# Kernel optimization log

Hardware: AMD Instinct MI355X
Metric: run time of the kernel (lower is better)

## Reference

```python
import jax, jax.numpy as jnp
import numpy as np

B, S = 32, 8192
HE, HD = 256, 256  # encoder_hidden_size, decoder_hidden_size


def setup_inputs() -> dict:
    key = jax.random.key(0)
    ks = jax.random.split(key, 8)
    scale = 1.0 / np.sqrt(HD)
    scale_e = 1.0 / np.sqrt(HE)
    return {
        "query": jax.random.normal(ks[0], (B, 1, HD), dtype=jnp.float32),
        "keys": jax.random.normal(ks[1], (B, S, HE), dtype=jnp.float32),
        "Wa_w": jax.random.uniform(ks[2], (HD, HD), jnp.float32, -scale, scale),
        "Wa_b": jax.random.uniform(ks[3], (HD,), jnp.float32, -scale, scale),
        "Ua_w": jax.random.uniform(ks[4], (HD, HE), jnp.float32, -scale_e, scale_e),
        "Ua_b": jax.random.uniform(ks[5], (HD,), jnp.float32, -scale_e, scale_e),
        "Va_w": jax.random.uniform(ks[6], (1, HD), jnp.float32, -scale, scale),
        "Va_b": jax.random.uniform(ks[7], (1,), jnp.float32, -scale, scale),
    }


def reference(query, keys, Wa_w, Wa_b, Ua_w, Ua_b, Va_w, Va_b):
    # q_proj: [B, 1, HD]; k_proj: [B, S, HD]
    q_proj = jnp.einsum("bqd,hd->bqh", query, Wa_w) + Wa_b
    k_proj = jnp.einsum("bse,he->bsh", keys, Ua_w) + Ua_b
    # scores: [B, S] -> [B, 1, S]
    scores = jnp.einsum("bsh,h->bs", jnp.tanh(q_proj + k_proj), Va_w[0]) + Va_b[0]
    weights = jax.nn.softmax(scores, axis=-1)[:, None, :]  # [B, 1, S]
    context = jnp.einsum("bqs,bse->bqe", weights, keys)    # [B, 1, HE]
    return (context, weights)
```

## Files before the change

### kernel.cpp

```cpp
#include <hip/hip_runtime.h>
#include <hip/hip_bf16.h>
#include <stdint.h>

#define B_ 32
#define S_ 8192
#define HD_ 256
#define HE_ 256
#define CHUNK 256
#define ROWS 16
#define MSTEPS (CHUNK/ROWS)
#define NCHUNK (S_/CHUNK)

typedef __attribute__((ext_vector_type(8))) short bf16x8;
typedef __attribute__((ext_vector_type(4))) float f32x4;

__device__ __forceinline__ uint32_t cvt_pk_bf16(float lo, float hi) {
  uint32_t r;
  asm("v_cvt_pk_bf16_f32 %0, %1, %2" : "=v"(r) : "v"(lo), "v"(hi));
  return r;
}
__device__ __forceinline__ float bf2f(unsigned short h) {
  return __uint_as_float(((uint32_t)h) << 16);
}
__device__ __forceinline__ float tanh_fast(float x) {
  float e = __expf(2.0f * x);
  return 1.0f - 2.0f * __builtin_amdgcn_rcpf(e + 1.0f);
}
template<int CTRL>
__device__ __forceinline__ float dpp_shr_add(float v) {
  int t = __builtin_amdgcn_update_dpp(0, __float_as_int(v), CTRL, 0xf, 0xf, true);
  return v + __int_as_float(t);
}
__device__ __forceinline__ float row16_sum(float v) {
  v = dpp_shr_add<0x118>(v);
  v = dpp_shr_add<0x114>(v);
  v = dpp_shr_add<0x112>(v);
  v = dpp_shr_add<0x111>(v);
  return v;
}

__global__ void prep_kernel(const float* __restrict__ query,
                            const float* __restrict__ Wa_w,
                            const float* __restrict__ Wa_b,
                            const float* __restrict__ Ua_w,
                            const float* __restrict__ Ua_b,
                            float* __restrict__ qv,
                            unsigned short* __restrict__ ua_bf) {
  const int blk = blockIdx.x, t = threadIdx.x;
  if (blk < B_) {
    __shared__ float qs[HD_];
    qs[t] = query[blk * HD_ + t];
    __syncthreads();
    const float* wr = Wa_w + (size_t)t * HD_;
    float s = Wa_b[t] + Ua_b[t];
#pragma unroll 8
    for (int d = 0; d < HD_; ++d) s += qs[d] * wr[d];
    qv[blk * HD_ + t] = s;
  } else {
    const int base = (blk - B_) * 2048 + t * 8;
    float4 v0 = *(const float4*)(Ua_w + base);
    float4 v1 = *(const float4*)(Ua_w + base + 4);
    uint4 pk;
    pk.x = cvt_pk_bf16(v0.x, v0.y);
    pk.y = cvt_pk_bf16(v0.z, v0.w);
    pk.z = cvt_pk_bf16(v1.x, v1.y);
    pk.w = cvt_pk_bf16(v1.z, v1.w);
    *(uint4*)(ua_bf + base) = pk;
  }
}

__global__ __launch_bounds__(512)
__attribute__((amdgpu_waves_per_eu(4, 4)))
void main_kernel(const float* __restrict__ keys,
                 const float* __restrict__ qv,
                 const float* __restrict__ Va_w,
                 const unsigned short* __restrict__ ua_bf,
                 float* __restrict__ wexp_g,
                 float* __restrict__ partials) {
  __shared__ __align__(16) char kt[2 * ROWS * 512];
  __shared__ float sc_sum[2][16];
  __shared__ __align__(16) float num_l[8][64][4];

  const int t = threadIdx.x;
  const int b = blockIdx.y;
  const int chunk = blockIdx.x;
  const int s0 = chunk * CHUNK;
  const int lane = t & 63;
  const int w = t >> 6;
  const int ln = lane & 15;
  const int hi = lane >> 4;

  const unsigned short* ub0 = ua_bf + (size_t)(w * 32 + ln) * HE_ + hi * 8;
  const unsigned short* ub1 = ub0 + 16 * HE_;
  bf16x8 bb0[8], bb1[8];
#pragma unroll
  for (int k = 0; k < 8; ++k) {
    bb0[k] = *(const bf16x8*)(ub0 + k * 32);
    bb1[k] = *(const bf16x8*)(ub1 + k * 32);
  }
  const float q0  = qv[b * HD_ + w * 32 + ln];
  const float q1  = qv[b * HD_ + w * 32 + 16 + ln];
  const float va0 = Va_w[w * 32 + ln];
  const float va1 = Va_w[w * 32 + 16 + ln];

  const int srow = t >> 5;
  const int scch = t & 31;
  const float* ksrc = keys + ((size_t)b * S_ + s0 + srow) * HE_ + scch * 8;
  const int ldsoff = srow * 512 + ((scch * 16) ^ ((srow & 7) << 4));

  if (t < 32) ((float*)sc_sum)[t] = 0.f;
  {
    float4 a0 = *(const float4*)(ksrc);
    float4 a1 = *(const float4*)(ksrc + 4);
    uint4 pk;
    pk.x = cvt_pk_bf16(a0.x, a0.y);
    pk.y = cvt_pk_bf16(a0.z, a0.w);
    pk.z = cvt_pk_bf16(a1.x, a1.y);
    pk.w = cvt_pk_bf16(a1.z, a1.w);
    *(uint4*)(kt + ldsoff) = pk;
  }
  __syncthreads();

  const int asw = (ln & 7) << 4;
  const int nsw = (w & 7) << 4;
  float num4[4] = {0.f, 0.f, 0.f, 0.f};

  for (int i = 0; i < MSTEPS; ++i) {
    char* cur = kt + (i & 1) * (ROWS * 512);
    char* nxt = kt + ((i + 1) & 1) * (ROWS * 512);

    float4 ga0, ga1;
    if (i + 1 < MSTEPS) {
      const float* kA = ksrc + (size_t)(i + 1) * ROWS * HE_;
      ga0 = *(const float4*)(kA);
      ga1 = *(const float4*)(kA + 4);
    }

    f32x4 a00 = {0.f,0.f,0.f,0.f}, a01 = {0.f,0.f,0.f,0.f};
    const char* arow = cur + ln * 512;
#pragma unroll
    for (int k = 0; k < 8; ++k) {
      bf16x8 af = *(const bf16x8*)(arow + ((k * 64 + hi * 16) ^ asw));
      a00 = __builtin_amdgcn_mfma_f32_16x16x32_bf16(af, bb0[k], a00, 0, 0, 0);
      a01 = __builtin_amdgcn_mfma_f32_16x16x32_bf16(af, bb1[k], a01, 0, 0, 0);
    }

#pragma unroll
    for (int r = 0; r < 4; ++r) {
      float v = tanh_fast(a00[r] + q0) * va0 + tanh_fast(a01[r] + q1) * va1;
      v = row16_sum(v);
      if (ln == 15) atomicAdd(&sc_sum[i & 1][hi * 4 + r], v);
    }
    __syncthreads();

    const float e0 = __expf(sc_sum[i & 1][w]);
    const float e8 = __expf(sc_sum[i & 1][w + 8]);
    if (lane == 0) {
      float* wg = wexp_g + (size_t)b * S_ + s0 + i * ROWS;
      wg[w] = e0;
      wg[w + 8] = e8;
    }
    if (t < 16) sc_sum[(i + 1) & 1][t] = 0.f;

    {
      uint2 kv0 = *(const uint2*)(cur + w * 512 + ((lane * 8) ^ nsw));
      uint2 kv1 = *(const uint2*)(cur + (w + 8) * 512 + ((lane * 8) ^ nsw));
      num4[0] += e0 * bf2f((unsigned short)(kv0.x & 0xffff)) + e8 * bf2f((unsigned short)(kv1.x & 0xffff));
      num4[1] += e0 * bf2f((unsigned short)(kv0.x >> 16))    + e8 * bf2f((unsigned short)(kv1.x >> 16));
      num4[2] += e0 * bf2f((unsigned short)(kv0.y & 0xffff)) + e8 * bf2f((unsigned short)(kv1.y & 0xffff));
      num4[3] += e0 * bf2f((unsigned short)(kv0.y >> 16))    + e8 * bf2f((unsigned short)(kv1.y >> 16));
    }

    if (i + 1 < MSTEPS) {
      uint4 pk;
      pk.x = cvt_pk_bf16(ga0.x, ga0.y);
      pk.y = cvt_pk_bf16(ga0.z, ga0.w);
      pk.z = cvt_pk_bf16(ga1.x, ga1.y);
      pk.w = cvt_pk_bf16(ga1.z, ga1.w);
      *(uint4*)(nxt + ldsoff) = pk;
    }
    __syncthreads();
  }

  *(float4*)&num_l[w][lane][0] = make_float4(num4[0], num4[1], num4[2], num4[3]);
  __syncthreads();
  if (t < 256) {
    float s = 0.f;
#pragma unroll
    for (int ww = 0; ww < 8; ++ww) s += num_l[ww][t >> 2][t & 3];
    partials[((size_t)b * NCHUNK + chunk) * 256 + t] = s;
  }
}

__global__ void combine_kernel(const float* __restrict__ wexp_g,
                               const float* __restrict__ partials,
                               float* __restrict__ out) {
  __shared__ float red[4];
  __shared__ float rdsh;
  const int b = blockIdx.x, t = threadIdx.x;
  const float* we = wexp_g + (size_t)b * S_;
  float s = 0.f;
#pragma unroll 4
  for (int i = t; i < S_; i += 256) s += we[i];
#pragma unroll
  for (int mm = 32; mm; mm >>= 1) s += __shfl_xor(s, mm, 64);
  if ((t & 63) == 0) red[t >> 6] = s;
  __syncthreads();
  if (t == 0) rdsh = 1.0f / (red[0] + red[1] + red[2] + red[3]);
  __syncthreads();
  const float rd = rdsh;

  const float* pb = partials + (size_t)b * NCHUNK * 256;
  float num = 0.f;
#pragma unroll 4
  for (int i = 0; i < NCHUNK; ++i) num += pb[i * 256 + t];
  out[b * HE_ + t] = num * rd;

  float* wout = out + B_ * HE_ + (size_t)b * S_;
#pragma unroll 4
  for (int i = t; i < S_; i += 256) wout[i] = we[i] * rd;
}

extern "C" void kernel_launch(void* const* d_in, const int* in_sizes, int n_in,
                              void* d_out, int out_size, void* d_ws, size_t ws_size,
                              hipStream_t stream) {
  const float* query = (const float*)d_in[0];
  const float* keys  = (const float*)d_in[1];
  const float* Wa_w  = (const float*)d_in[2];
  const float* Wa_b  = (const float*)d_in[3];
  const float* Ua_w  = (const float*)d_in[4];
  const float* Ua_b  = (const float*)d_in[5];
  const float* Va_w  = (const float*)d_in[6];
  float* out = (float*)d_out;

  char* ws = (char*)d_ws;
  float* qv             = (float*)ws;
  unsigned short* ua_bf = (unsigned short*)(ws + 32 * 1024);
  float* wexp_g         = (float*)(ws + 160 * 1024);
  float* partials       = (float*)(ws + 160 * 1024 + 1048576);

  prep_kernel<<<64, 256, 0, stream>>>(query, Wa_w, Wa_b, Ua_w, Ua_b, qv, ua_bf);
  dim3 g(NCHUNK, B_);
  main_kernel<<<g, 512, 0, stream>>>(keys, qv, Va_w, ua_bf, wexp_g, partials);
  combine_kernel<<<B_, 256, 0, stream>>>(wexp_g, partials, out);
}
```

Measured before the change: 85.00 us.

## Halve main kernel block to 4 waves, each covering 64 hidden columns

The main kernel now runs 256 threads (4 waves) per block instead of 512. Each wave holds four B-fragment sets (64 hidden units) in registers and issues four MFMAs per k-step. Each thread loads two key rows per step, and each wave handles four rows in the context accumulation. The aim is to amortise each LDS A-fragment read over more MFMAs and cut per-block sync overhead, at the cost of higher register pressure (64 bf16x8 B registers) and possibly lower occupancy.

```diff
diff --git a/kernel.cpp b/kernel.cpp
--- a/kernel.cpp
+++ b/kernel.cpp
@@ -69,8 +69,7 @@
   }
 }
 
-__global__ __launch_bounds__(512)
-__attribute__((amdgpu_waves_per_eu(4, 4)))
+__global__ __launch_bounds__(256, 2)
 void main_kernel(const float* __restrict__ keys,
                  const float* __restrict__ qv,
                  const float* __restrict__ Va_w,
@@ -79,7 +78,7 @@
                  float* __restrict__ partials) {
   __shared__ __align__(16) char kt[2 * ROWS * 512];
   __shared__ float sc_sum[2][16];
-  __shared__ __align__(16) float num_l[8][64][4];
+  __shared__ __align__(16) float num_l[4][64][4];
 
   const int t = threadIdx.x;
   const int b = blockIdx.y;
@@ -90,85 +89,109 @@
   const int ln = lane & 15;
   const int hi = lane >> 4;
 
-  const unsigned short* ub0 = ua_bf + (size_t)(w * 32 + ln) * HE_ + hi * 8;
-  const unsigned short* ub1 = ub0 + 16 * HE_;
-  bf16x8 bb0[8], bb1[8];
+  const unsigned short* ub = ua_bf + (size_t)(w * 64 + ln) * HE_ + hi * 8;
+  bf16x8 bb0[8], bb1[8], bb2[8], bb3[8];
 #pragma unroll
   for (int k = 0; k < 8; ++k) {
-    bb0[k] = *(const bf16x8*)(ub0 + k * 32);
-    bb1[k] = *(const bf16x8*)(ub1 + k * 32);
-  }
-  const float q0  = qv[b * HD_ + w * 32 + ln];
-  const float q1  = qv[b * HD_ + w * 32 + 16 + ln];
-  const float va0 = Va_w[w * 32 + ln];
-  const float va1 = Va_w[w * 32 + 16 + ln];
+    bb0[k] = *(const bf16x8*)(ub + k * 32);
+    bb1[k] = *(const bf16x8*)(ub + 16 * HE_ + k * 32);
+    bb2[k] = *(const bf16x8*)(ub + 32 * HE_ + k * 32);
+    bb3[k] = *(const bf16x8*)(ub + 48 * HE_ + k * 32);
+  }
+  const int hbase = b * HD_ + w * 64 + ln;
+  const float q0  = qv[hbase];
+  const float q1  = qv[hbase + 16];
+  const float q2  = qv[hbase + 32];
+  const float q3  = qv[hbase + 48];
+  const float va0 = Va_w[w * 64 + ln];
+  const float va1 = Va_w[w * 64 + 16 + ln];
+  const float va2 = Va_w[w * 64 + 32 + ln];
+  const float va3 = Va_w[w * 64 + 48 + ln];
 
   const int srow = t >> 5;
   const int scch = t & 31;
-  const float* ksrc = keys + ((size_t)b * S_ + s0 + srow) * HE_ + scch * 8;
-  const int ldsoff = srow * 512 + ((scch * 16) ^ ((srow & 7) << 4));
+  const float* ksrcA = keys + ((size_t)b * S_ + s0 + srow) * HE_ + scch * 8;
+  const float* ksrcB = ksrcA + 8 * HE_;
+  const int ldsoffA = srow * 512 + ((scch * 16) ^ ((srow & 7) << 4));
+  const int ldsoffB = ldsoffA + 8 * 512;
 
   if (t < 32) ((float*)sc_sum)[t] = 0.f;
   {
-    float4 a0 = *(const float4*)(ksrc);
-    float4 a1 = *(const float4*)(ksrc + 4);
+    float4 a0 = *(const float4*)(ksrcA);
+    float4 a1 = *(const float4*)(ksrcA + 4);
+    float4 c0 = *(const float4*)(ksrcB);
+    float4 c1 = *(const float4*)(ksrcB + 4);
     uint4 pk;
     pk.x = cvt_pk_bf16(a0.x, a0.y);
     pk.y = cvt_pk_bf16(a0.z, a0.w);
     pk.z = cvt_pk_bf16(a1.x, a1.y);
     pk.w = cvt_pk_bf16(a1.z, a1.w);
-    *(uint4*)(kt + ldsoff) = pk;
+    *(uint4*)(kt + ldsoffA) = pk;
+    pk.x = cvt_pk_bf16(c0.x, c0.y);
+    pk.y = cvt_pk_bf16(c0.z, c0.w);
+    pk.z = cvt_pk_bf16(c1.x, c1.y);
+    pk.w = cvt_pk_bf16(c1.z, c1.w);
+    *(uint4*)(kt + ldsoffB) = pk;
   }
   __syncthreads();
 
   const int asw = (ln & 7) << 4;
-  const int nsw = (w & 7) << 4;
   float num4[4] = {0.f, 0.f, 0.f, 0.f};
 
   for (int i = 0; i < MSTEPS; ++i) {
     char* cur = kt + (i & 1) * (ROWS * 512);
     char* nxt = kt + ((i + 1) & 1) * (ROWS * 512);
 
-    float4 ga0, ga1;
+    float4 ga0, ga1, gc0, gc1;
     if (i + 1 < MSTEPS) {
-      const float* kA = ksrc + (size_t)(i + 1) * ROWS * HE_;
+      const float* kA = ksrcA + (size_t)(i + 1) * ROWS * HE_;
+      const float* kB = ksrcB + (size_t)(i + 1) * ROWS * HE_;
       ga0 = *(const float4*)(kA);
       ga1 = *(const float4*)(kA + 4);
-    }
-
-    f32x4 a00 = {0.f,0.f,0.f,0.f}, a01 = {0.f,0.f,0.f,0.f};
+      gc0 = *(const float4*)(kB);
+      gc1 = *(const float4*)(kB + 4);
+    }
+
+    f32x4 a0 = {0.f,0.f,0.f,0.f}, a1 = {0.f,0.f,0.f,0.f};
+    f32x4 a2 = {0.f,0.f,0.f,0.f}, a3 = {0.f,0.f,0.f,0.f};
     const char* arow = cur + ln * 512;
 #pragma unroll
     for (int k = 0; k < 8; ++k) {
       bf16x8 af = *(const bf16x8*)(arow + ((k * 64 + hi * 16) ^ asw));
-      a00 = __builtin_amdgcn_mfma_f32_16x16x32_bf16(af, bb0[k], a00, 0, 0, 0);
-      a01 = __builtin_amdgcn_mfma_f32_16x16x32_bf16(af, bb1[k], a01, 0, 0, 0);
+      a0 = __builtin_amdgcn_mfma_f32_16x16x32_bf16(af, bb0[k], a0, 0, 0, 0);
+      a1 = __builtin_amdgcn_mfma_f32_16x16x32_bf16(af, bb1[k], a1, 0, 0, 0);
+      a2 = __builtin_amdgcn_mfma_f32_16x16x32_bf16(af, bb2[k], a2, 0, 0, 0);
+      a3 = __builtin_amdgcn_mfma_f32_16x16x32_bf16(af, bb3[k], a3, 0, 0, 0);
     }
 
 #pragma unroll
     for (int r = 0; r < 4; ++r) {
-      float v = tanh_fast(a00[r] + q0) * va0 + tanh_fast(a01[r] + q1) * va1;
+      float v = tanh_fast(a0[r] + q0) * va0 + tanh_fast(a1[r] + q1) * va1
+              + tanh_fast(a2[r] + q2) * va2 + tanh_fast(a3[r] + q3) * va3;
       v = row16_sum(v);
       if (ln == 15) atomicAdd(&sc_sum[i & 1][hi * 4 + r], v);
     }
     __syncthreads();
 
-    const float e0 = __expf(sc_sum[i & 1][w]);
-    const float e8 = __expf(sc_sum[i & 1][w + 8]);
+    const float e0 = __expf(sc_sum[i & 1][4 * w + 0]);
+    const float e1 = __expf(sc_sum[i & 1][4 * w + 1]);
+    const float e2 = __expf(sc_sum[i & 1][4 * w + 2]);
+    const float e3 = __expf(sc_sum[i & 1][4 * w + 3]);
     if (lane == 0) {
-      float* wg = wexp_g + (size_t)b * S_ + s0 + i * ROWS;
-      wg[w] = e0;
-      wg[w + 8] = e8;
+      float* wg = wexp_g + (size_t)b * S_ + s0 + i * ROWS + 4 * w;
+      wg[0] = e0; wg[1] = e1; wg[2] = e2; wg[3] = e3;
     }
     if (t < 16) sc_sum[(i + 1) & 1][t] = 0.f;
 
-    {
-      uint2 kv0 = *(const uint2*)(cur + w * 512 + ((lane * 8) ^ nsw));
-      uint2 kv1 = *(const uint2*)(cur + (w + 8) * 512 + ((lane * 8) ^ nsw));
-      num4[0] += e0 * bf2f((unsigned short)(kv0.x & 0xffff)) + e8 * bf2f((unsigned short)(kv1.x & 0xffff));
-      num4[1] += e0 * bf2f((unsigned short)(kv0.x >> 16))    + e8 * bf2f((unsigned short)(kv1.x >> 16));
-      num4[2] += e0 * bf2f((unsigned short)(kv0.y & 0xffff)) + e8 * bf2f((unsigned short)(kv1.y & 0xffff));
-      num4[3] += e0 * bf2f((unsigned short)(kv0.y >> 16))    + e8 * bf2f((unsigned short)(kv1.y >> 16));
+#pragma unroll
+    for (int j = 0; j < 4; ++j) {
+      const int row = 4 * w + j;
+      const float e = (j == 0) ? e0 : (j == 1) ? e1 : (j == 2) ? e2 : e3;
+      uint2 kv = *(const uint2*)(cur + row * 512 + ((lane * 8) ^ ((row & 7) << 4)));
+      num4[0] += e * bf2f((unsigned short)(kv.x & 0xffff));
+      num4[1] += e * bf2f((unsigned short)(kv.x >> 16));
+      num4[2] += e * bf2f((unsigned short)(kv.y & 0xffff));
+      num4[3] += e * bf2f((unsigned short)(kv.y >> 16));
     }
 
     if (i + 1 < MSTEPS) {
@@ -177,17 +200,22 @@
       pk.y = cvt_pk_bf16(ga0.z, ga0.w);
       pk.z = cvt_pk_bf16(ga1.x, ga1.y);
       pk.w = cvt_pk_bf16(ga1.z, ga1.w);
-      *(uint4*)(nxt + ldsoff) = pk;
+      *(uint4*)(nxt + ldsoffA) = pk;
+      pk.x = cvt_pk_bf16(gc0.x, gc0.y);
+      pk.y = cvt_pk_bf16(gc0.z, gc0.w);
+      pk.z = cvt_pk_bf16(gc1.x, gc1.y);
+      pk.w = cvt_pk_bf16(gc1.z, gc1.w);
+      *(uint4*)(nxt + ldsoffB) = pk;
     }
     __syncthreads();
   }
 
   *(float4*)&num_l[w][lane][0] = make_float4(num4[0], num4[1], num4[2], num4[3]);
   __syncthreads();
-  if (t < 256) {
+  {
     float s = 0.f;
 #pragma unroll
-    for (int ww = 0; ww < 8; ++ww) s += num_l[ww][t >> 2][t & 3];
+    for (int ww = 0; ww < 4; ++ww) s += num_l[ww][t >> 2][t & 3];
     partials[((size_t)b * NCHUNK + chunk) * 256 + t] = s;
   }
 }
@@ -241,6 +269,6 @@
 
   prep_kernel<<<64, 256, 0, stream>>>(query, Wa_w, Wa_b, Ua_w, Ua_b, qv, ua_bf);
   dim3 g(NCHUNK, B_);
-  main_kernel<<<g, 512, 0, stream>>>(keys, qv, Va_w, ua_bf, wexp_g, partials);
+  main_kernel<<<g, 256, 0, stream>>>(keys, qv, Va_w, ua_bf, wexp_g, partials);
   combine_kernel<<<B_, 256, 0, stream>>>(wexp_g, partials, out);
 }
```

Result: no change. 85.30 us (+0.3%).

## Software-pipeline score exp and context accumulation one step behind MFMA

Applied to the files above, without the earlier changes.

Restructures the main loop so the softmax exponentials and weighted key accumulation for step i-1 run in the same phase as the MFMA/tanh scoring for step i, removing one __syncthreads per iteration. To make this safe it uses a 4-deep LDS tile ring and a 3-slot score buffer, plus an epilogue for the last step. This adds LDS usage and loop complexity in exchange for fewer barriers.

```diff
diff --git a/kernel.cpp b/kernel.cpp
--- a/kernel.cpp
+++ b/kernel.cpp
@@ -10,6 +10,7 @@
 #define ROWS 16
 #define MSTEPS (CHUNK/ROWS)
 #define NCHUNK (S_/CHUNK)
+#define TILE (ROWS * 512)
 
 typedef __attribute__((ext_vector_type(8))) short bf16x8;
 typedef __attribute__((ext_vector_type(4))) float f32x4;
@@ -77,8 +78,8 @@
                  const unsigned short* __restrict__ ua_bf,
                  float* __restrict__ wexp_g,
                  float* __restrict__ partials) {
-  __shared__ __align__(16) char kt[2 * ROWS * 512];
-  __shared__ float sc_sum[2][16];
+  __shared__ __align__(16) char kt[4 * TILE];
+  __shared__ float sc3[3][16];
   __shared__ __align__(16) float num_l[8][64][4];
 
   const int t = threadIdx.x;
@@ -108,7 +109,7 @@
   const float* ksrc = keys + ((size_t)b * S_ + s0 + srow) * HE_ + scch * 8;
   const int ldsoff = srow * 512 + ((scch * 16) ^ ((srow & 7) << 4));
 
-  if (t < 32) ((float*)sc_sum)[t] = 0.f;
+  if (t < 48) ((float*)sc3)[t] = 0.f;
   {
     float4 a0 = *(const float4*)(ksrc);
     float4 a1 = *(const float4*)(ksrc + 4);
@@ -126,8 +127,9 @@
   float num4[4] = {0.f, 0.f, 0.f, 0.f};
 
   for (int i = 0; i < MSTEPS; ++i) {
-    char* cur = kt + (i & 1) * (ROWS * 512);
-    char* nxt = kt + ((i + 1) & 1) * (ROWS * 512);
+    char* cur = kt + (i & 3) * TILE;
+    char* stg = kt + ((i + 1) & 3) * TILE;
+    char* prv = kt + ((i + 3) & 3) * TILE;
 
     float4 ga0, ga1;
     if (i + 1 < MSTEPS) {
@@ -145,31 +147,31 @@
       a01 = __builtin_amdgcn_mfma_f32_16x16x32_bf16(af, bb1[k], a01, 0, 0, 0);
     }
 
-#pragma unroll
-    for (int r = 0; r < 4; ++r) {
-      float v = tanh_fast(a00[r] + q0) * va0 + tanh_fast(a01[r] + q1) * va1;
-      v = row16_sum(v);
-      if (ln == 15) atomicAdd(&sc_sum[i & 1][hi * 4 + r], v);
-    }
-    __syncthreads();
-
-    const float e0 = __expf(sc_sum[i & 1][w]);
-    const float e8 = __expf(sc_sum[i & 1][w + 8]);
-    if (lane == 0) {
-      float* wg = wexp_g + (size_t)b * S_ + s0 + i * ROWS;
-      wg[w] = e0;
-      wg[w + 8] = e8;
-    }
-    if (t < 16) sc_sum[(i + 1) & 1][t] = 0.f;
-
-    {
-      uint2 kv0 = *(const uint2*)(cur + w * 512 + ((lane * 8) ^ nsw));
-      uint2 kv1 = *(const uint2*)(cur + (w + 8) * 512 + ((lane * 8) ^ nsw));
+    if (i > 0) {
+      const float* scp = sc3[(i + 2) % 3];
+      const float e0 = __expf(scp[w]);
+      const float e8 = __expf(scp[w + 8]);
+      if (lane == 0) {
+        float* wg = wexp_g + (size_t)b * S_ + s0 + (i - 1) * ROWS;
+        wg[w] = e0;
+        wg[w + 8] = e8;
+      }
+      uint2 kv0 = *(const uint2*)(prv + w * 512 + ((lane * 8) ^ nsw));
+      uint2 kv1 = *(const uint2*)(prv + (w + 8) * 512 + ((lane * 8) ^ nsw));
       num4[0] += e0 * bf2f((unsigned short)(kv0.x & 0xffff)) + e8 * bf2f((unsigned short)(kv1.x & 0xffff));
       num4[1] += e0 * bf2f((unsigned short)(kv0.x >> 16))    + e8 * bf2f((unsigned short)(kv1.x >> 16));
       num4[2] += e0 * bf2f((unsigned short)(kv0.y & 0xffff)) + e8 * bf2f((unsigned short)(kv1.y & 0xffff));
       num4[3] += e0 * bf2f((unsigned short)(kv0.y >> 16))    + e8 * bf2f((unsigned short)(kv1.y >> 16));
     }
+
+#pragma unroll
+    for (int r = 0; r < 4; ++r) {
+      float v = tanh_fast(a00[r] + q0) * va0 + tanh_fast(a01[r] + q1) * va1;
+      v = row16_sum(v);
+      if (ln == 15) atomicAdd(&sc3[i % 3][hi * 4 + r], v);
+    }
+
+    if (t < 16) sc3[(i + 1) % 3][t] = 0.f;
 
     if (i + 1 < MSTEPS) {
       uint4 pk;
@@ -177,9 +179,27 @@
       pk.y = cvt_pk_bf16(ga0.z, ga0.w);
       pk.z = cvt_pk_bf16(ga1.x, ga1.y);
       pk.w = cvt_pk_bf16(ga1.z, ga1.w);
-      *(uint4*)(nxt + ldsoff) = pk;
+      *(uint4*)(stg + ldsoff) = pk;
     }
     __syncthreads();
+  }
+
+  {
+    const float* scp = sc3[(MSTEPS - 1) % 3];
+    const char* prv = kt + ((MSTEPS - 1) & 3) * TILE;
+    const float e0 = __expf(scp[w]);
+    const float e8 = __expf(scp[w + 8]);
+    if (lane == 0) {
+      float* wg = wexp_g + (size_t)b * S_ + s0 + (MSTEPS - 1) * ROWS;
+      wg[w] = e0;
+      wg[w + 8] = e8;
+    }
+    uint2 kv0 = *(const uint2*)(prv + w * 512 + ((lane * 8) ^ nsw));
+    uint2 kv1 = *(const uint2*)(prv + (w + 8) * 512 + ((lane * 8) ^ nsw));
+    num4[0] += e0 * bf2f((unsigned short)(kv0.x & 0xffff)) + e8 * bf2f((unsigned short)(kv1.x & 0xffff));
+    num4[1] += e0 * bf2f((unsigned short)(kv0.x >> 16))    + e8 * bf2f((unsigned short)(kv1.x >> 16));
+    num4[2] += e0 * bf2f((unsigned short)(kv0.y & 0xffff)) + e8 * bf2f((unsigned short)(kv1.y & 0xffff));
+    num4[3] += e0 * bf2f((unsigned short)(kv0.y >> 16))    + e8 * bf2f((unsigned short)(kv1.y >> 16));
   }
 
   *(float4*)&num_l[w][lane][0] = make_float4(num4[0], num4[1], num4[2], num4[3]);
```

Result: faster. 81.05 us (-4.6%).
